# Kernel tuning notes

Hardware: AMD Instinct MI355X
Metric: run time of the kernel (lower is better)

The kernel has to match this reference:

```python
import jax, jax.numpy as jnp
import numpy as np

B, S, D_IN, D_MODEL, H = 4, 2048, 1024, 1024, 16
HD = D_MODEL // H  # 64


def setup_inputs() -> dict:
    key = jax.random.key(0)
    k1, k2, k3, k4, k5 = jax.random.split(key, 5)
    x = jax.random.normal(k1, (B, S, D_IN), dtype=jnp.float32)
    mask = jnp.zeros((1, 1, S, S), dtype=jnp.float32)  # additive mask
    # qkv_layer: Linear(D_IN, 3*D_MODEL)
    W_qkv = jax.random.normal(k2, (D_IN, 3 * D_MODEL), dtype=jnp.float32) / np.sqrt(D_IN)
    b_qkv = jax.random.normal(k3, (3 * D_MODEL,), dtype=jnp.float32) * 0.01
    # linear_layer: Linear(D_MODEL, D_MODEL)
    W_o = jax.random.normal(k4, (D_MODEL, D_MODEL), dtype=jnp.float32) / np.sqrt(D_MODEL)
    b_o = jax.random.normal(k5, (D_MODEL,), dtype=jnp.float32) * 0.01
    return {"x": x, "mask": mask, "W_qkv": W_qkv, "b_qkv": b_qkv, "W_o": W_o, "b_o": b_o}


def reference(x, mask, W_qkv, b_qkv, W_o, b_o):
    b, s, _ = x.shape
    qkv = x @ W_qkv + b_qkv                                  # [B,S,3*D]
    qkv = qkv.reshape(b, s, H, 3 * HD).transpose(0, 2, 1, 3)  # [B,H,S,3*HD]
    q, k, v = jnp.split(qkv, 3, axis=-1)                     # each [B,H,S,HD]
    scale = 1.0 / jnp.sqrt(jnp.asarray(HD, dtype=q.dtype))
    scores = jnp.einsum('bhqd,bhkd->bhqk', q, k) * scale + mask  # [B,H,S,S]
    attn = jax.nn.softmax(scores, axis=-1)
    values = jnp.einsum('bhqk,bhkd->bhqd', attn, v)           # [B,H,S,HD]
    values = values.transpose(0, 2, 1, 3).reshape(b, s, H * HD)  # [B,S,D]
    out = values @ W_o + b_o
    return (out, values)
```

## Files before the change

kernel.cpp:

```cpp
#include <hip/hip_runtime.h>
#include <hip/hip_bf16.h>


typedef __attribute__((ext_vector_type(8))) short short8;
typedef __attribute__((ext_vector_type(4))) float f32x4;

#define SCL2E 0.1803368801111204f
#define L2E   1.44269504088896340736f

#define GLD16(g, l)                                                            \
  __builtin_amdgcn_global_load_lds(                                            \
      (const __attribute__((address_space(1))) unsigned int*)(g),              \
      (__attribute__((address_space(3))) unsigned int*)(l), 16, 0, 0)

__device__ __forceinline__ unsigned short f2b(float f) {
  union { float f; unsigned int u; } v; v.f = f;
  unsigned int u = v.u;
  return (unsigned short)((u + 0x7fffu + ((u >> 16) & 1u)) >> 16);
}
__device__ __forceinline__ unsigned int fbits(float f) {
  union { float f; unsigned int u; } v; v.f = f; return v.u;
}
__device__ __forceinline__ unsigned int cvt_pk_bf16(float lo, float hi) {
  unsigned int r;
  asm("v_cvt_pk_bf16_f32 %0, %1, %2" : "=v"(r) : "v"(lo), "v"(hi));
  return r;
}

__global__ void cvt_bf16(const float* __restrict__ in, ushort* __restrict__ out,
                         int n, unsigned int* __restrict__ mflags) {
  if (blockIdx.x == 0 && threadIdx.x < 16) mflags[threadIdx.x] = 0u;
  int i = (blockIdx.x * blockDim.x + threadIdx.x) * 4;
  if (i + 3 < n) {
    float4 f = *(const float4*)(in + i);
    ushort4 o;
    o.x = f2b(f.x); o.y = f2b(f.y); o.z = f2b(f.z); o.w = f2b(f.w);
    *(ushort4*)(out + i) = o;
  }
}

__global__ void mask_flags_k(const float* __restrict__ mask,
                             unsigned int* __restrict__ mflags) {
  __shared__ unsigned int s;
  const int qt = blockIdx.x >> 4, kt = blockIdx.x & 15;
  const float* base = mask + (size_t)(qt * 128) * 2048 + kt * 128;
  const int row = threadIdx.x >> 1, col0 = (threadIdx.x & 1) * 64;
  unsigned int acc = 0;
#pragma unroll
  for (int i = 0; i < 16; ++i) {
    float4 f = *(const float4*)(base + (size_t)row * 2048 + col0 + i * 4);
    acc |= fbits(f.x) | fbits(f.y) | fbits(f.z) | fbits(f.w);
  }
  acc &= 0x7fffffffu;
  if (threadIdx.x == 0) s = 0u;
  __syncthreads();
  if (acc) atomicOr(&s, 1u);
  __syncthreads();
  if (threadIdx.x == 0 && s) atomicOr(&mflags[qt], 1u << kt);
}

__global__ void transpose_cvt(const float* __restrict__ W, ushort* __restrict__ Wt,
                              int K, int N) {
  __shared__ float tile[64][65];
  int n0 = blockIdx.x * 64, k0 = blockIdx.y * 64;
  int tx = threadIdx.x & 63, ty = threadIdx.x >> 6;
#pragma unroll
  for (int i = 0; i < 64; i += 4)
    tile[ty + i][tx] = W[(size_t)(k0 + ty + i) * N + n0 + tx];
  __syncthreads();
#pragma unroll
  for (int i = 0; i < 64; i += 4)
    Wt[(size_t)(n0 + ty + i) * K + k0 + tx] = f2b(tile[tx][ty + i]);
}

template <int OUTF32, int QSCALE>
__global__ __launch_bounds__(256, 2) void gemm_bt_bias(
    const ushort* __restrict__ A, const ushort* __restrict__ Bt,
    const float* __restrict__ bias, void* __restrict__ Cout,
    int M, int N, int K) {
  __shared__ ushort As[128 * 64];
  __shared__ ushort Bs[128 * 64];
  const int lane = threadIdx.x & 63;
  const int wv = threadIdx.x >> 6;
  const int bm = blockIdx.y, bn = blockIdx.x;
  const int wm = wv >> 1, wn = wv & 1;
  f32x4 acc[4][4] = {};
  const size_t arow0 = (size_t)bm * 128;
  const size_t brow0 = (size_t)bn * 128;

  for (int k0 = 0; k0 < K; k0 += 64) {
    __syncthreads();
#pragma unroll
    for (int i = 0; i < 4; ++i) {
      int r = wv * 32 + i * 8 + (lane >> 3);
      const ushort* ga = A + (arow0 + r) * K + k0 + (lane & 7) * 8;
      GLD16(ga, As + (wv * 32 + i * 8) * 64);
      const ushort* gb = Bt + (brow0 + r) * K + k0 + (lane & 7) * 8;
      GLD16(gb, Bs + (wv * 32 + i * 8) * 64);
    }
    __syncthreads();
    short8 af[2][4], bf[2][4];
#pragma unroll
    for (int kf = 0; kf < 2; ++kf)
#pragma unroll
      for (int t = 0; t < 4; ++t) {
        af[kf][t] = *(const short8*)(As + (wm * 64 + t * 16 + (lane & 15)) * 64 +
                                     kf * 32 + (lane >> 4) * 8);
        bf[kf][t] = *(const short8*)(Bs + (wn * 64 + t * 16 + (lane & 15)) * 64 +
                                     kf * 32 + (lane >> 4) * 8);
      }
#pragma unroll
    for (int kf = 0; kf < 2; ++kf)
#pragma unroll
      for (int mt = 0; mt < 4; ++mt)
#pragma unroll
        for (int nt = 0; nt < 4; ++nt)
          acc[mt][nt] = __builtin_amdgcn_mfma_f32_16x16x32_bf16(
              af[kf][mt], bf[kf][nt], acc[mt][nt], 0, 0, 0);
  }
#pragma unroll
  for (int nt = 0; nt < 4; ++nt) {
    int col = bn * 128 + wn * 64 + nt * 16 + (lane & 15);
    float bv = bias[col];
    float scl = (QSCALE && (col % 192) < 64) ? SCL2E : 1.0f;
#pragma unroll
    for (int mt = 0; mt < 4; ++mt) {
      int row0 = bm * 128 + wm * 64 + mt * 16 + (lane >> 4) * 4;
#pragma unroll
      for (int r = 0; r < 4; ++r) {
        float v = acc[mt][nt][r] + bv;
        if (QSCALE) v *= scl;
        if (OUTF32)
          ((float*)Cout)[(size_t)(row0 + r) * N + col] = v;
        else
          ((ushort*)Cout)[(size_t)(row0 + r) * N + col] = f2b(v);
      }
    }
  }
}

__global__ __launch_bounds__(256, 2) void flash_attn(
    const ushort* __restrict__ qkv, const float* __restrict__ mask,
    const unsigned int* __restrict__ mflags,
    float* __restrict__ values_f, ushort* __restrict__ values_b) {
  __shared__ ushort Ks[2][128 * 64];
  __shared__ ushort Vt[64 * 136];

  const int lane = threadIdx.x & 63;
  const int wv = threadIdx.x >> 6;
  const int c = lane & 15;
  const int g = lane >> 4;
  const int bh = blockIdx.x & 63;
  const int qt = blockIdx.x >> 6;
  const int b = bh >> 4, h = bh & 15;
  const size_t rowbase = (size_t)b * 2048;
  const int qcol = h * 192;
  const int swz = (c & 3) << 1;
  const unsigned int flbits = mflags[qt];

  const short8 vone = {0x3F80, 0x3F80, 0x3F80, 0x3F80,
                       0x3F80, 0x3F80, 0x3F80, 0x3F80};

  short8 qf[2][2];
#pragma unroll
  for (int mt = 0; mt < 2; ++mt)
#pragma unroll
    for (int kf = 0; kf < 2; ++kf)
      qf[mt][kf] = *(const short8*)(qkv +
          (rowbase + qt * 128 + wv * 32 + mt * 16 + c) * 3072 + qcol +
          kf * 32 + g * 8);

  f32x4 acc[2][4] = {};
  f32x4 accl[2] = {};
  float mst[2] = {-3e38f, -3e38f};

  const int K0 = lane * 2;
  const int dq = wv;
  const int pc0 = ((K0 >> 5) << 5) + (((K0 >> 2) & 3) << 3) +
                  (((K0 >> 4) & 1) << 2) + (K0 & 3);
  const int vdw = pc0 >> 1;
  const int gcol = (((lane & 7) ^ (((lane >> 3) & 3) << 1)) << 3);

  short8 va0, va1, vb0, vb1;

  auto loadV = [&](int t) {
    const ushort* vg = qkv + (rowbase + t * 128 + K0) * 3072 + qcol + 128 + dq * 16;
    va0 = *(const short8*)(vg);
    va1 = *(const short8*)(vg + 8);
    vb0 = *(const short8*)(vg + 3072);
    vb1 = *(const short8*)(vg + 3072 + 8);
  };
  auto writeV = [&]() {
    unsigned int* Vdw = (unsigned int*)Vt;
#pragma unroll
    for (int j = 0; j < 8; ++j)
      Vdw[(dq * 16 + j) * 68 + vdw] =
          ((unsigned int)(unsigned short)vb0[j] << 16) | (unsigned short)va0[j];
#pragma unroll
    for (int j = 0; j < 8; ++j)
      Vdw[(dq * 16 + 8 + j) * 68 + vdw] =
          ((unsigned int)(unsigned short)vb1[j] << 16) | (unsigned short)va1[j];
  };
  auto stageK = [&](int t, ushort* KsD) {
#pragma unroll
    for (int i = 0; i < 4; ++i) {
      int rloc = wv * 32 + i * 8;
      const ushort* gk = qkv + (rowbase + t * 128 + rloc + (lane >> 3)) * 3072 +
                         qcol + 64 + gcol;
      GLD16(gk, KsD + rloc * 64);
    }
  };

  const float* mrow = mask + (size_t)(qt * 128 + wv * 32 + c) * 2048 + g * 4;

  loadV(0);
  stageK(0, Ks[0]);
  writeV();

  for (int kt = 0; kt < 16; ++kt) {
    __syncthreads();
    const int cur = kt & 1;
    const ushort* KsC = Ks[cur];
    if (kt < 15) {
      loadV(kt + 1);
      stageK(kt + 1, Ks[cur ^ 1]);
    }

    const bool hasmask = (flbits >> kt) & 1u;
    const float* mkt = mrow + kt * 128;
    float4 msk0[8];
    if (hasmask) {
#pragma unroll
      for (int nt = 0; nt < 8; ++nt) msk0[nt] = *(const float4*)(mkt + nt * 16);
    }

    f32x4 sc[2][8];
    __builtin_amdgcn_s_setprio(1);
#pragma unroll
    for (int nt = 0; nt < 8; ++nt) {
      short8 k0 = *(const short8*)(KsC + (nt * 16 + c) * 64 + ((g ^ swz) << 3));
      short8 k1 = *(const short8*)(KsC + (nt * 16 + c) * 64 + (((4 + g) ^ swz) << 3));
      f32x4 z = {0.f, 0.f, 0.f, 0.f};
      sc[0][nt] = __builtin_amdgcn_mfma_f32_16x16x32_bf16(k0, qf[0][0], z, 0, 0, 0);
      sc[0][nt] = __builtin_amdgcn_mfma_f32_16x16x32_bf16(k1, qf[0][1], sc[0][nt], 0, 0, 0);
      sc[1][nt] = __builtin_amdgcn_mfma_f32_16x16x32_bf16(k0, qf[1][0], z, 0, 0, 0);
      sc[1][nt] = __builtin_amdgcn_mfma_f32_16x16x32_bf16(k1, qf[1][1], sc[1][nt], 0, 0, 0);
    }
    __builtin_amdgcn_s_setprio(0);

    __attribute__((aligned(16))) unsigned int Dw[2][16];
#pragma unroll
    for (int mt = 0; mt < 2; ++mt) {
      f32x4 t4[8];
      if (hasmask) {
#pragma unroll
        for (int nt = 0; nt < 8; ++nt) {
          float4 mk = (mt == 0) ? msk0[nt]
                                : *(const float4*)(mkt + 16 * 2048 + nt * 16);
#pragma unroll
          for (int r = 0; r < 4; ++r)
            t4[nt][r] = fmaf(((const float*)&mk)[r], L2E, sc[mt][nt][r]);
        }
      } else {
#pragma unroll
        for (int nt = 0; nt < 8; ++nt) t4[nt] = sc[mt][nt];
      }
      f32x4 vm = t4[0];
#pragma unroll
      for (int nt = 1; nt < 8; ++nt)
#pragma unroll
        for (int r = 0; r < 4; ++r) vm[r] = fmaxf(vm[r], t4[nt][r]);
      float pm = fmaxf(fmaxf(vm[0], vm[1]), fmaxf(vm[2], vm[3]));
      pm = fmaxf(pm, __shfl_xor(pm, 16));
      pm = fmaxf(pm, __shfl_xor(pm, 32));
      if (!__all(pm <= mst[mt] + 8.0f)) {
        float mnew = fmaxf(mst[mt], pm);
        float alpha = exp2f(mst[mt] - mnew);
        mst[mt] = mnew;
#pragma unroll
        for (int dt = 0; dt < 4; ++dt)
#pragma unroll
          for (int r = 0; r < 4; ++r) acc[mt][dt][r] *= alpha;
#pragma unroll
        for (int r = 0; r < 4; ++r) accl[mt][r] *= alpha;
      }
      const float mcur = mst[mt];
#pragma unroll
      for (int nt = 0; nt < 8; ++nt) {
        float p0 = exp2f(t4[nt][0] - mcur);
        float p1 = exp2f(t4[nt][1] - mcur);
        float p2 = exp2f(t4[nt][2] - mcur);
        float p3 = exp2f(t4[nt][3] - mcur);
        Dw[mt][nt * 2 + 0] = cvt_pk_bf16(p0, p1);
        Dw[mt][nt * 2 + 1] = cvt_pk_bf16(p2, p3);
      }
    }

    const short8* bu0 = (const short8*)Dw[0];
    const short8* bu1 = (const short8*)Dw[1];
    __builtin_amdgcn_s_setprio(1);
#pragma unroll
    for (int dt = 0; dt < 4; ++dt)
#pragma unroll
      for (int kf = 0; kf < 4; ++kf) {
        short8 vf = *(const short8*)(Vt + (dt * 16 + c) * 136 + kf * 32 + g * 8);
        acc[0][dt] = __builtin_amdgcn_mfma_f32_16x16x32_bf16(vf, bu0[kf], acc[0][dt], 0, 0, 0);
        acc[1][dt] = __builtin_amdgcn_mfma_f32_16x16x32_bf16(vf, bu1[kf], acc[1][dt], 0, 0, 0);
      }
#pragma unroll
    for (int kf = 0; kf < 4; ++kf) {
      accl[0] = __builtin_amdgcn_mfma_f32_16x16x32_bf16(vone, bu0[kf], accl[0], 0, 0, 0);
      accl[1] = __builtin_amdgcn_mfma_f32_16x16x32_bf16(vone, bu1[kf], accl[1], 0, 0, 0);
    }
    __builtin_amdgcn_s_setprio(0);

    if (kt < 15) {
      __syncthreads();
      writeV();
    }
  }

#pragma unroll
  for (int mt = 0; mt < 2; ++mt) {
    float rl = 1.0f / accl[mt][0];
    size_t qrow = rowbase + qt * 128 + wv * 32 + mt * 16 + c;
#pragma unroll
    for (int dt = 0; dt < 4; ++dt) {
      int d0 = h * 64 + dt * 16 + g * 4;
      float4 o;
      o.x = acc[mt][dt][0] * rl; o.y = acc[mt][dt][1] * rl;
      o.z = acc[mt][dt][2] * rl; o.w = acc[mt][dt][3] * rl;
      *(float4*)(values_f + qrow * 1024 + d0) = o;
      ushort4 ob;
      ob.x = f2b(o.x); ob.y = f2b(o.y); ob.z = f2b(o.z); ob.w = f2b(o.w);
      *(ushort4*)(values_b + qrow * 1024 + d0) = ob;
    }
  }
}

extern "C" void kernel_launch(void* const* d_in, const int* in_sizes, int n_in,
                              void* d_out, int out_size, void* d_ws, size_t ws_size,
                              hipStream_t stream) {
  const float* x    = (const float*)d_in[0];
  const float* mask = (const float*)d_in[1];
  const float* Wqkv = (const float*)d_in[2];
  const float* bqkv = (const float*)d_in[3];
  const float* Wo   = (const float*)d_in[4];
  const float* bo   = (const float*)d_in[5];
  float* out      = (float*)d_out;
  float* values_f = out + 8388608;

  char* ws = (char*)d_ws;
  ushort* xb    = (ushort*)(ws + 0);
  ushort* wqkvt = (ushort*)(ws + 16777216);
  ushort* wot   = (ushort*)(ws + 23068672);
  ushort* qkv   = (ushort*)(ws + 25165824);
  ushort* valb  = (ushort*)(ws + 75497472);
  unsigned int* mflg = (unsigned int*)(ws + 92274688);

  cvt_bf16<<<dim3(8192), dim3(256), 0, stream>>>(x, xb, 8388608, mflg);
  mask_flags_k<<<dim3(256), dim3(256), 0, stream>>>(mask, mflg);
  transpose_cvt<<<dim3(48, 16), dim3(256), 0, stream>>>(Wqkv, wqkvt, 1024, 3072);
  transpose_cvt<<<dim3(16, 16), dim3(256), 0, stream>>>(Wo, wot, 1024, 1024);
  gemm_bt_bias<0, 1><<<dim3(24, 64), dim3(256), 0, stream>>>(
      xb, wqkvt, bqkv, (void*)qkv, 8192, 3072, 1024);
  flash_attn<<<dim3(1024), dim3(256), 0, stream>>>(qkv, mask, mflg, values_f, valb);
  gemm_bt_bias<1, 0><<<dim3(8, 64), dim3(256), 0, stream>>>(
      valb, wot, bo, (void*)out, 8192, 1024, 1024);
}
```

Before: 356.0 us.

## Merge prep kernels, split attention launch, skip rescale and tune softmax math

Folds the x conversion and mask-flag scan into one prep kernel and the two weight transposes into one launch, so the prologue makes fewer kernel launches. Mask flags become per-tile bytes that each block writes directly, which removes the atomics and the flag zeroing. In attention, V packing uses byte-permute instructions, the row max uses three-input max, and the running max starts at zero with a wider lazy-rescale window and a cheaper exp path when the max is still zero. The attention grid is also split into two launches of half the query tiles. The wider threshold allows larger unnormalized exponent values, a small accuracy and overflow risk.

```diff
diff --git a/kernel.cpp b/kernel.cpp
--- a/kernel.cpp
+++ b/kernel.cpp
@@ -26,23 +26,25 @@
   asm("v_cvt_pk_bf16_f32 %0, %1, %2" : "=v"(r) : "v"(lo), "v"(hi));
   return r;
 }
-
-__global__ void cvt_bf16(const float* __restrict__ in, ushort* __restrict__ out,
-                         int n, unsigned int* __restrict__ mflags) {
-  if (blockIdx.x == 0 && threadIdx.x < 16) mflags[threadIdx.x] = 0u;
-  int i = (blockIdx.x * blockDim.x + threadIdx.x) * 4;
-  if (i + 3 < n) {
+__device__ __forceinline__ float max3f(float a, float b, float c) {
+  return fmaxf(fmaxf(a, b), c);
+}
+
+__global__ void prep(const float* __restrict__ in, ushort* __restrict__ out,
+                     const float* __restrict__ mask,
+                     unsigned char* __restrict__ mflagsB) {
+  const int bid = blockIdx.x;
+  if (bid < 8192) {
+    int i = (bid * 256 + threadIdx.x) * 4;
     float4 f = *(const float4*)(in + i);
     ushort4 o;
     o.x = f2b(f.x); o.y = f2b(f.y); o.z = f2b(f.z); o.w = f2b(f.w);
     *(ushort4*)(out + i) = o;
-  }
-}
-
-__global__ void mask_flags_k(const float* __restrict__ mask,
-                             unsigned int* __restrict__ mflags) {
+    return;
+  }
   __shared__ unsigned int s;
-  const int qt = blockIdx.x >> 4, kt = blockIdx.x & 15;
+  const int t = bid - 8192;
+  const int qt = t >> 4, kt = t & 15;
   const float* base = mask + (size_t)(qt * 128) * 2048 + kt * 128;
   const int row = threadIdx.x >> 1, col0 = (threadIdx.x & 1) * 64;
   unsigned int acc = 0;
@@ -56,13 +58,17 @@
   __syncthreads();
   if (acc) atomicOr(&s, 1u);
   __syncthreads();
-  if (threadIdx.x == 0 && s) atomicOr(&mflags[qt], 1u << kt);
-}
-
-__global__ void transpose_cvt(const float* __restrict__ W, ushort* __restrict__ Wt,
-                              int K, int N) {
+  if (threadIdx.x == 0) mflagsB[t] = s ? 1 : 0;
+}
+
+__global__ void transpose_cvt2(const float* __restrict__ W1, ushort* __restrict__ Wt1,
+                               const float* __restrict__ W2, ushort* __restrict__ Wt2) {
   __shared__ float tile[64][65];
-  int n0 = blockIdx.x * 64, k0 = blockIdx.y * 64;
+  const int bx = blockIdx.x;
+  const float* W; ushort* Wt; int N, n0;
+  if (bx < 48) { W = W1; Wt = Wt1; N = 3072; n0 = bx * 64; }
+  else         { W = W2; Wt = Wt2; N = 1024; n0 = (bx - 48) * 64; }
+  const int K = 1024, k0 = blockIdx.y * 64;
   int tx = threadIdx.x & 63, ty = threadIdx.x >> 6;
 #pragma unroll
   for (int i = 0; i < 64; i += 4)
@@ -141,8 +147,8 @@
 
 __global__ __launch_bounds__(256, 2) void flash_attn(
     const ushort* __restrict__ qkv, const float* __restrict__ mask,
-    const unsigned int* __restrict__ mflags,
-    float* __restrict__ values_f, ushort* __restrict__ values_b) {
+    const unsigned char* __restrict__ mflagsB,
+    float* __restrict__ values_f, ushort* __restrict__ values_b, int qoff) {
   __shared__ ushort Ks[2][128 * 64];
   __shared__ ushort Vt[64 * 136];
 
@@ -151,12 +157,18 @@
   const int c = lane & 15;
   const int g = lane >> 4;
   const int bh = blockIdx.x & 63;
-  const int qt = blockIdx.x >> 6;
+  const int qt = (blockIdx.x >> 6) + qoff;
   const int b = bh >> 4, h = bh & 15;
   const size_t rowbase = (size_t)b * 2048;
   const int qcol = h * 192;
   const int swz = (c & 3) << 1;
-  const unsigned int flbits = mflags[qt];
+
+  unsigned int flbits = 0;
+  {
+    const unsigned char* mb = mflagsB + qt * 16;
+#pragma unroll
+    for (int i = 0; i < 16; ++i) flbits |= (mb[i] ? 1u : 0u) << i;
+  }
 
   const short8 vone = {0x3F80, 0x3F80, 0x3F80, 0x3F80,
                        0x3F80, 0x3F80, 0x3F80, 0x3F80};
@@ -172,7 +184,7 @@
 
   f32x4 acc[2][4] = {};
   f32x4 accl[2] = {};
-  float mst[2] = {-3e38f, -3e38f};
+  float mst[2] = {0.f, 0.f};
 
   const int K0 = lane * 2;
   const int dq = wv;
@@ -192,14 +204,24 @@
   };
   auto writeV = [&]() {
     unsigned int* Vdw = (unsigned int*)Vt;
-#pragma unroll
-    for (int j = 0; j < 8; ++j)
-      Vdw[(dq * 16 + j) * 68 + vdw] =
-          ((unsigned int)(unsigned short)vb0[j] << 16) | (unsigned short)va0[j];
-#pragma unroll
-    for (int j = 0; j < 8; ++j)
-      Vdw[(dq * 16 + 8 + j) * 68 + vdw] =
-          ((unsigned int)(unsigned short)vb1[j] << 16) | (unsigned short)va1[j];
+    const unsigned int* aw0 = (const unsigned int*)&va0;
+    const unsigned int* bw0 = (const unsigned int*)&vb0;
+    const unsigned int* aw1 = (const unsigned int*)&va1;
+    const unsigned int* bw1 = (const unsigned int*)&vb1;
+#pragma unroll
+    for (int k = 0; k < 4; ++k) {
+      Vdw[(dq * 16 + 2 * k + 0) * 68 + vdw] =
+          __builtin_amdgcn_perm(bw0[k], aw0[k], 0x05040100u);
+      Vdw[(dq * 16 + 2 * k + 1) * 68 + vdw] =
+          __builtin_amdgcn_perm(bw0[k], aw0[k], 0x07060302u);
+    }
+#pragma unroll
+    for (int k = 0; k < 4; ++k) {
+      Vdw[(dq * 16 + 8 + 2 * k + 0) * 68 + vdw] =
+          __builtin_amdgcn_perm(bw1[k], aw1[k], 0x05040100u);
+      Vdw[(dq * 16 + 8 + 2 * k + 1) * 68 + vdw] =
+          __builtin_amdgcn_perm(bw1[k], aw1[k], 0x07060302u);
+    }
   };
   auto stageK = [&](int t, ushort* KsD) {
 #pragma unroll
@@ -265,17 +287,22 @@
 #pragma unroll
         for (int nt = 0; nt < 8; ++nt) t4[nt] = sc[mt][nt];
       }
-      f32x4 vm = t4[0];
-#pragma unroll
-      for (int nt = 1; nt < 8; ++nt)
-#pragma unroll
-        for (int r = 0; r < 4; ++r) vm[r] = fmaxf(vm[r], t4[nt][r]);
-      float pm = fmaxf(fmaxf(vm[0], vm[1]), fmaxf(vm[2], vm[3]));
+      f32x4 u, v, w, vm;
+#pragma unroll
+      for (int r = 0; r < 4; ++r) {
+        u[r] = max3f(t4[0][r], t4[1][r], t4[2][r]);
+        v[r] = max3f(t4[3][r], t4[4][r], t4[5][r]);
+        w[r] = max3f(t4[6][r], t4[7][r], u[r]);
+        vm[r] = fmaxf(v[r], w[r]);
+      }
+      float pm = fmaxf(max3f(vm[0], vm[1], vm[2]), vm[3]);
       pm = fmaxf(pm, __shfl_xor(pm, 16));
       pm = fmaxf(pm, __shfl_xor(pm, 32));
-      if (!__all(pm <= mst[mt] + 8.0f)) {
+      if (!__all(pm <= mst[mt] + 16.0f && pm >= mst[mt] - 40.0f)) {
         float mnew = fmaxf(mst[mt], pm);
-        float alpha = exp2f(mst[mt] - mnew);
+        bool fresh = (accl[mt][0] == 0.0f);
+        if (fresh) mnew = pm;
+        float alpha = fresh ? 0.0f : exp2f(mst[mt] - mnew);
         mst[mt] = mnew;
 #pragma unroll
         for (int dt = 0; dt < 4; ++dt)
@@ -284,15 +311,22 @@
 #pragma unroll
         for (int r = 0; r < 4; ++r) accl[mt][r] *= alpha;
       }
-      const float mcur = mst[mt];
+      if (__any(mst[mt] != 0.0f)) {
+        const float mcur = mst[mt];
+#pragma unroll
+        for (int nt = 0; nt < 8; ++nt)
+#pragma unroll
+          for (int r = 0; r < 4; ++r) t4[nt][r] = exp2f(t4[nt][r] - mcur);
+      } else {
+#pragma unroll
+        for (int nt = 0; nt < 8; ++nt)
+#pragma unroll
+          for (int r = 0; r < 4; ++r) t4[nt][r] = exp2f(t4[nt][r]);
+      }
 #pragma unroll
       for (int nt = 0; nt < 8; ++nt) {
-        float p0 = exp2f(t4[nt][0] - mcur);
-        float p1 = exp2f(t4[nt][1] - mcur);
-        float p2 = exp2f(t4[nt][2] - mcur);
-        float p3 = exp2f(t4[nt][3] - mcur);
-        Dw[mt][nt * 2 + 0] = cvt_pk_bf16(p0, p1);
-        Dw[mt][nt * 2 + 1] = cvt_pk_bf16(p2, p3);
+        Dw[mt][nt * 2 + 0] = cvt_pk_bf16(t4[nt][0], t4[nt][1]);
+        Dw[mt][nt * 2 + 1] = cvt_pk_bf16(t4[nt][2], t4[nt][3]);
       }
     }
 
@@ -356,15 +390,14 @@
   ushort* wot   = (ushort*)(ws + 23068672);
   ushort* qkv   = (ushort*)(ws + 25165824);
   ushort* valb  = (ushort*)(ws + 75497472);
-  unsigned int* mflg = (unsigned int*)(ws + 92274688);
-
-  cvt_bf16<<<dim3(8192), dim3(256), 0, stream>>>(x, xb, 8388608, mflg);
-  mask_flags_k<<<dim3(256), dim3(256), 0, stream>>>(mask, mflg);
-  transpose_cvt<<<dim3(48, 16), dim3(256), 0, stream>>>(Wqkv, wqkvt, 1024, 3072);
-  transpose_cvt<<<dim3(16, 16), dim3(256), 0, stream>>>(Wo, wot, 1024, 1024);
+  unsigned char* mflg = (unsigned char*)(ws + 92274688);
+
+  prep<<<dim3(8448), dim3(256), 0, stream>>>(x, xb, mask, mflg);
+  transpose_cvt2<<<dim3(64, 16), dim3(256), 0, stream>>>(Wqkv, wqkvt, Wo, wot);
   gemm_bt_bias<0, 1><<<dim3(24, 64), dim3(256), 0, stream>>>(
       xb, wqkvt, bqkv, (void*)qkv, 8192, 3072, 1024);
-  flash_attn<<<dim3(1024), dim3(256), 0, stream>>>(qkv, mask, mflg, values_f, valb);
+  flash_attn<<<dim3(512), dim3(256), 0, stream>>>(qkv, mask, mflg, values_f, valb, 0);
+  flash_attn<<<dim3(512), dim3(256), 0, stream>>>(qkv, mask, mflg, values_f, valb, 8);
   gemm_bt_bias<1, 0><<<dim3(8, 64), dim3(256), 0, stream>>>(
       valb, wot, bo, (void*)out, 8192, 1024, 1024);
 }
```

Measured after the change: 361.1 us. Within noise of the previous version (+1.4%).
